# Kernel tuning notes

Hardware: AMD Instinct MI355X
Metric: run time of the kernel (lower is better)

## Reference

```python
import jax, jax.numpy as jnp
import numpy as np

B, D, L = 16, 256, 200
T = 1000   # max_frame_length
K = 3      # kernel_size
DW, DC = 4, 2


def setup_inputs() -> dict:
    key = jax.random.key(0)
    ks = jax.random.split(key, 16)
    plen = jax.random.randint(ks[0], (B,), 150, L + 1)
    pm = jnp.arange(L)[None, :] < plen[:, None]              # (B,L) True=valid
    phoneme_mask = pm[:, None, :]                            # (B,1,L)
    durations = jax.random.uniform(ks[1], (B, L), minval=1.0, maxval=8.0) * pm
    phoneme = jax.random.normal(ks[2], (B, D, L), dtype=jnp.float32)
    s = 0.05
    params = {
        'Wpw': jax.random.normal(ks[3], (D, D)) * s, 'bpw': jnp.zeros((D,)),
        'Cw': jax.random.normal(ks[4], (8, D, K)) * s, 'cbw': jnp.zeros((8,)),
        'Mw': jax.random.normal(ks[5], (10, DW)) * s, 'mbw': jnp.zeros((DW,)),
        'Lw': jax.random.normal(ks[6], (DW * D, D)) * s, 'lbw': jnp.zeros((D,)),
        'Wpc': jax.random.normal(ks[7], (D, D)) * s, 'bpc': jnp.zeros((D,)),
        'Cc': jax.random.normal(ks[8], (8, D, K)) * s, 'cbc': jnp.zeros((8,)),
        'Mc': jax.random.normal(ks[9], (10, DC)) * s, 'mbc': jnp.zeros((DC,)),
        'Lc': jax.random.normal(ks[10], (DW * DC, D)) * s, 'lbc': jnp.zeros((D,)),
        'Wo': jax.random.normal(ks[11], (D, 2 * D)) * s, 'bo': jnp.zeros((2 * D,)),
    }
    return {'durations': durations, 'phoneme': phoneme, 'phoneme_mask': phoneme_mask, **params}


def _conv_swish(x, W1, b1, Ck, cb, pm):
    # 1x1 conv (proj) then kernel-K 'same' conv then SiLU; mask padded phones
    h = jnp.einsum('od,bdl->bol', W1, x) + b1[None, :, None]
    h = jax.lax.conv_general_dilated(h, Ck, (1,), 'SAME',
                                     dimension_numbers=('NCH', 'OIH', 'NCH')) + cb[None, :, None]
    h = jax.nn.silu(h)
    h = jnp.where(pm[:, None, :], h, 0.0)
    return h.transpose(0, 2, 1)  # (B, L, 8)


def _mlp(S, E, h, M, mb):
    # concat start/end boundary scalars with per-phone conv features -> (B,T,L,10)
    feat = jnp.concatenate([S[..., None], E[..., None],
                            jnp.broadcast_to(h[:, None], (B, T, L, 8))], axis=-1)
    return jax.nn.silu(feat @ M + mb)


def _forward(durations, phoneme, phoneme_mask, Wpw, bpw, Cw, cbw, Mw, mbw, Lw, lbw,
             Wpc, bpc, Cc, cbc, Mc, mbc, Lc, lbc, Wo, bo):
    pm = phoneme_mask[:, 0, :]                                          # (B,L)
    frame_lengths = jnp.clip(jnp.round(durations.sum(-1)).astype(jnp.int32), 0, T)
    frame_mask = jnp.arange(T)[None, :] < frame_lengths[:, None]        # (B,T)
    attn_mask = frame_mask[:, :, None] & pm[:, None, :]                 # (B,T,L)
    sd = jnp.cumsum(durations, axis=-1)                                 # (B,L)
    sk = sd - durations
    t = jnp.arange(1, T + 1, dtype=durations.dtype)
    S = jnp.where(attn_mask, t[None, :, None] - sk[:, None, :], 0.0)    # (B,T,L)
    E = jnp.where(attn_mask, (sd - sk)[:, None, :], 0.0)                # (B,T,L)

    h_w = _conv_swish(phoneme, Wpw, bpw, Cw, cbw, pm)
    w = _mlp(S, E, h_w, Mw, mbw)                                        # (B,T,L,DW)
    w = jnp.where(pm[:, None, :, None], w, -jnp.inf)
    w = jax.nn.softmax(w, axis=2)                                       # softmax over phones
    w = jnp.where(frame_mask[:, :, None, None], w, 0.0)

    h_c = _conv_swish(phoneme, Wpc, bpc, Cc, cbc, pm)
    c = _mlp(S, E, h_c, Mc, mbc)                                        # (B,T,L,DC)

    wh = jnp.einsum('btlq,bdl->btqd', w, phoneme).reshape(B, T, DW * D) @ Lw + lbw
    wc = jnp.einsum('btlq,btlp->btqp', w, c).reshape(B, T, DW * DC) @ Lc + lbc
    whc = jnp.where(frame_mask[..., None], wh + wc, 0.0)                # (B,T,D)
    out = (whc @ Wo + bo).transpose(0, 2, 1)                            # (B,2D,T)
    return out, frame_mask, frame_lengths, w.transpose(0, 3, 1, 2)


def reference(durations, phoneme, phoneme_mask, Wpw, bpw, Cw, cbw, Mw, mbw, Lw, lbw,
              Wpc, bpc, Cc, cbc, Mc, mbc, Lc, lbc, Wo, bo):
    out, frame_mask, frame_lengths, w = _forward(
        durations, phoneme, phoneme_mask, Wpw, bpw, Cw, cbw, Mw, mbw, Lw, lbw,
        Wpc, bpc, Cc, cbc, Mc, mbc, Lc, lbc, Wo, bo)
    mean, log_std = jnp.split(out, 2, axis=1)                           # (B,D,T) each
    return (mean, log_std, frame_mask, frame_lengths, w)
```

## Files before the change

### kernel.cpp

```cpp
#include <hip/hip_runtime.h>
#include <hip/hip_bf16.h>
#include <math.h>

#define NB 16
#define ND 256
#define NL 200
#define NT 1000

typedef unsigned short ushort_t;
typedef __bf16 bf16x8 __attribute__((ext_vector_type(8)));
typedef float f32x4 __attribute__((ext_vector_type(4)));

#define LDS_AS(p) ((__attribute__((address_space(3))) void*)(p))
#define GLB_AS(p) ((const __attribute__((address_space(1))) void*)(p))

#define OFF_PHT   0u
#define OFF_SK    4966400u
#define OFF_EW    4969600u
#define OFF_EC    4975744u
#define OFF_BW2   4981888u
#define OFF_BC2   4981912u
#define OFF_FL    4981936u
#define OFF_GT    11535552u
#define OFF_WOT   15221952u
#define OFF_BASE  15287488u
#define OFF_PHTB  15320256u
#define OFF_LWT   15844544u

__device__ __forceinline__ float silu_f(float x){ return x / (1.f + __expf(-x)); }
__device__ __forceinline__ ushort_t f2bf(float x){
  __hip_bfloat16 h = __float2bfloat16(x);
  return *(ushort_t*)&h;
}

__global__ __launch_bounds__(256) void k_stage1(
    const float* __restrict__ dur, const float* __restrict__ ph,
    const float* __restrict__ Wp_w, const float* __restrict__ C_w, const float* __restrict__ bp_w,
    const float* __restrict__ Wp_c, const float* __restrict__ C_c, const float* __restrict__ bp_c,
    const float* __restrict__ Wo, const float* __restrict__ Lw,
    float* __restrict__ sk_ws, int* __restrict__ fl_ws,
    float* __restrict__ o_fm, float* __restrict__ o_fl,
    float* __restrict__ Ew, float* __restrict__ Ec,
    float* __restrict__ bw2, float* __restrict__ bc2,
    ushort_t* __restrict__ WoT, ushort_t* __restrict__ LwT,
    float* __restrict__ phT, ushort_t* __restrict__ phTb)
{
  int bid = blockIdx.x, tid = threadIdx.x;
  if (bid < 16){
    int b = bid;
    __shared__ float sdur[NL];
    __shared__ float ssk[NL];
    __shared__ int sfl;
    if (tid < NL) sdur[tid] = dur[b*NL + tid];
    __syncthreads();
    if (tid == 0){
      float run = 0.f;
      for (int l = 0; l < NL; ++l){ ssk[l] = run; run += sdur[l]; }
      int fl = (int)rintf(run);
      fl = fl < 0 ? 0 : (fl > NT ? NT : fl);
      sfl = fl; fl_ws[b] = fl; o_fl[b] = (float)fl;
    }
    __syncthreads();
    if (tid < NL) sk_ws[b*NL + tid] = ssk[tid];
    for (int t = tid; t < NT; t += 256) o_fm[b*NT + t] = (t < sfl) ? 1.f : 0.f;
  } else if (bid < 1600){
    int sbid = bid - 16;
    if (sbid < 48){
      int gid = sbid*256 + tid;
      int branch = gid / 6144;
      int r = gid % 6144;
      int d = r & 255;
      int ock = r >> 8;
      int oc = ock / 3, k = ock % 3;
      const float* Wp = branch ? Wp_c : Wp_w;
      const float* C  = branch ? C_c  : C_w;
      float acc = 0.f;
      for (int i = 0; i < ND; ++i) acc += C[(oc*ND + i)*3 + k] * Wp[i*ND + d];
      (branch ? Ec : Ew)[r] = acc;
      if (d == 0){
        const float* bp = branch ? bp_c : bp_w;
        float bb = 0.f;
        for (int i = 0; i < ND; ++i) bb += C[(oc*ND + i)*3 + k] * bp[i];
        (branch ? bc2 : bw2)[ock] = bb;
      }
    } else {
      int gid = (sbid - 48)*256 + tid;
      if (gid < 131072){
        int n = gid >> 8, k = gid & 255;
        WoT[gid] = f2bf(Wo[(size_t)k*512 + n]);
      } else {
        int r = gid - 131072;
        int d = r & 255;
        int qn = r >> 8;
        int q = qn >> 8, n = qn & 255;
        LwT[r] = f2bf(Lw[((size_t)q*256 + d)*256 + n]);
      }
    }
  } else {
    int r = bid - 1600;
    int xb = r & 7, yb = (r >> 3) & 7, b = r >> 6;
    int l0 = xb*32, d0 = yb*32;
    int tx = tid & 31, ty = tid >> 5;
    __shared__ float tile[32][33];
    #pragma unroll
    for (int i = 0; i < 4; ++i){
      int d = d0 + ty + i*8, l = l0 + tx;
      tile[ty + i*8][tx] = (l < NL) ? ph[((size_t)b*ND + d)*NL + l] : 0.f;
    }
    __syncthreads();
    #pragma unroll
    for (int i = 0; i < 4; ++i){
      int l = l0 + ty + i*8, d = d0 + tx;
      float v = tile[tx][ty + i*8];
      if (l < NL) phT[((size_t)b*NL + l)*ND + d] = v;
      phTb[((size_t)b*256 + l)*ND + d] = f2bf(v);
    }
  }
}

__global__ __launch_bounds__(256) void k_stage2(
    const float* __restrict__ phT,
    const float* __restrict__ dur, const float* __restrict__ sk_ws,
    const float* __restrict__ Ew, const float* __restrict__ Ec,
    const float* __restrict__ bw2, const float* __restrict__ bc2,
    const float* __restrict__ cbw, const float* __restrict__ cbc,
    const float* __restrict__ Mw, const float* __restrict__ mbw,
    const float* __restrict__ Mc, const float* __restrict__ mbc,
    float4* __restrict__ base,
    const ushort_t* __restrict__ LwT, const ushort_t* __restrict__ phTb,
    ushort_t* __restrict__ Gt)
{
  int bid = blockIdx.x, tid = threadIdx.x;
  if (bid < 256){
    int b = bid >> 4, x = bid & 15;
    if (x >= 13){
      int l0 = 208 + (x - 13)*16;
      if (tid < 32)
        base[((size_t)(b*256 + l0 + (tid >> 1)))*2 + (tid & 1)] = make_float4(0,0,0,0);
      return;
    }
    __shared__ float sh[16][17];
    int lu = tid >> 4, u = tid & 15;
    int l = x*16 + lu;
    float h = 0.f;
    if (l < NL){
      int branch = u >> 3, oc = u & 7;
      const float* E  = branch ? Ec  : Ew;
      const float* b2 = branch ? bc2 : bw2;
      float val = (branch ? cbc : cbw)[oc];
      #pragma unroll
      for (int k = 0; k < 3; ++k){
        int ll = l + k - 1;
        if (ll < 0 || ll >= NL) continue;
        float acc = b2[oc*3 + k];
        const float4* Er = (const float4*)(E + (oc*3 + k)*ND);
        const float4* pr = (const float4*)(phT + ((size_t)b*NL + ll)*ND);
        #pragma unroll 8
        for (int d = 0; d < 64; ++d){
          float4 e = Er[d], p = pr[d];
          acc += e.x*p.x + e.y*p.y + e.z*p.z + e.w*p.w;
        }
        val += acc;
      }
      float pm = (dur[b*NL + l] > 0.5f) ? 1.f : 0.f;
      h = silu_f(val) * pm;
    }
    sh[lu][u] = h;
    __syncthreads();
    if (tid < 16){
      int ll = x*16 + tid;
      float4 o0 = make_float4(0,0,0,0);
      float4 o1 = make_float4(0,0,0,0);
      if (ll < NL){
        float dl  = dur[b*NL + ll];
        float pm  = (dl > 0.5f) ? 1.f : 0.f;
        float skl = sk_ws[b*NL + ll];
        float c1[4], c2[2];
        #pragma unroll
        for (int q = 0; q < 4; ++q) c1[q] = mbw[q] + dl*Mw[4 + q] - skl*Mw[q];
        #pragma unroll
        for (int p = 0; p < 2; ++p) c2[p] = mbc[p] + dl*Mc[2 + p] - skl*Mc[p];
        #pragma unroll
        for (int j = 0; j < 8; ++j){
          float hwv = sh[tid][j], hcv = sh[tid][8 + j];
          #pragma unroll
          for (int q = 0; q < 4; ++q) c1[q] += hwv*Mw[(2 + j)*4 + q];
          #pragma unroll
          for (int p = 0; p < 2; ++p) c2[p] += hcv*Mc[(2 + j)*2 + p];
        }
        o0 = make_float4(c1[0], c1[1], c1[2], c1[3]);
        o1 = make_float4(c2[0], c2[1], pm, 0.f);
      }
      base[((size_t)(b*256 + ll))*2 + 0] = o0;
      base[((size_t)(b*256 + ll))*2 + 1] = o1;
    }
  } else {
    int r = bid - 256;
    int xb = r & 1, yb = (r >> 1) & 1, bq = r >> 2;
    int b = bq >> 2, q = bq & 3;
    int m0 = yb * 128;
    int n0 = xb * 128;
    __shared__ ushort_t As[4096];
    __shared__ ushort_t Bs[4096];
    int lane = tid & 63, wave = tid >> 6;
    int wm = wave >> 1, wn = wave & 1;
    int col = lane & 15, kg4 = lane >> 4;
    f32x4 acc[4][4] = {};
    for (int kt = 0; kt < 8; ++kt){
      int k0 = kt*32;
      #pragma unroll
      for (int rr = 0; rr < 2; ++rr){
        int o = wave*1024 + rr*4096;
        int co = o + (lane << 4);
        int kg = co >> 11, row = (co >> 4) & 127;
        const ushort_t* ga = LwT + ((size_t)(q*256 + m0 + row))*256 + k0 + kg*8;
        __builtin_amdgcn_global_load_lds(GLB_AS(ga), LDS_AS(As + (o >> 1)), 16, 0, 0);
        const ushort_t* gb = phTb + ((size_t)(b*256 + n0 + row))*256 + k0 + kg*8;
        __builtin_amdgcn_global_load_lds(GLB_AS(gb), LDS_AS(Bs + (o >> 1)), 16, 0, 0);
      }
      __builtin_amdgcn_s_waitcnt(0);
      __syncthreads();
      const bf16x8* Av = (const bf16x8*)As;
      const bf16x8* Bv = (const bf16x8*)Bs;
      bf16x8 afr[4], bfr[4];
      #pragma unroll
      for (int i = 0; i < 4; ++i) afr[i] = Av[kg4*128 + wm*64 + i*16 + col];
      #pragma unroll
      for (int j = 0; j < 4; ++j) bfr[j] = Bv[kg4*128 + wn*64 + j*16 + col];
      #pragma unroll
      for (int i = 0; i < 4; ++i)
        #pragma unroll
        for (int j = 0; j < 4; ++j)
          acc[i][j] = __builtin_amdgcn_mfma_f32_16x16x32_bf16(afr[i], bfr[j], acc[i][j], 0, 0, 0);
      __syncthreads();
    }
    int rq = lane >> 4;
    #pragma unroll
    for (int i = 0; i < 4; ++i){
      #pragma unroll
      for (int rr = 0; rr < 4; ++rr){
        int n = m0 + wm*64 + i*16 + rq*4 + rr;
        #pragma unroll
        for (int j = 0; j < 4; ++j){
          int l = n0 + wn*64 + j*16 + col;
          if (l < NL)
            Gt[((size_t)b*ND + n)*800 + q*NL + l] = f2bf(acc[i][j][rr]);
        }
      }
    }
  }
}

#define AP 808
#define WP 264
__global__ __launch_bounds__(256) void k_wvo(
    const float4* __restrict__ base,
    const int* __restrict__ fl_ws,
    const float* __restrict__ Mw, const float* __restrict__ Mc,
    const ushort_t* __restrict__ Gt,
    const ushort_t* __restrict__ WoT,
    const float* __restrict__ Lc,
    const float* __restrict__ lbc,
    const float* __restrict__ lbw,
    const float* __restrict__ bo,
    float* __restrict__ wout,
    float* __restrict__ o_mean, float* __restrict__ o_lstd)
{
  __shared__ ushort_t As[16*AP];
  __shared__ ushort_t Bs[8192];
  __shared__ ushort_t whcs[16*WP];
  __shared__ float    wcs[16][8];
  int b = blockIdx.y;
  int m0 = blockIdx.x * 16;
  int tid = threadIdx.x, lane = tid & 63, wave = tid >> 6;
  int col = lane & 15, kg4 = lane >> 4, quad = lane >> 4;
  int fl = fl_ws[b];

  for (int s = 0; s < 4; ++s){
    int tl = wave*4 + s;
    int t = m0 + tl;
    if (t >= fl){
      for (int k = lane; k < 800; k += 64) As[tl*AP + k] = 0;
      if (lane < 8) wcs[tl][lane] = 0.f;
      if (t < NT){
        #pragma unroll
        for (int q = 0; q < 4; ++q)
          #pragma unroll
          for (int c = 0; c < 4; ++c){
            int l = c*64 + lane;
            if (l < NL) wout[(((size_t)(b*4 + q))*NT + t)*NL + l] = 0.f;
          }
      }
      continue;
    }
    float t1 = (float)(t + 1);
    float tqw[4], tqc[2];
    #pragma unroll
    for (int q = 0; q < 4; ++q) tqw[q] = t1 * Mw[q];
    #pragma unroll
    for (int p = 0; p < 2; ++p) tqc[p] = t1 * Mc[p];
    float z[4][4], cv[4][2], msk[4];
    float m[4] = {-INFINITY, -INFINITY, -INFINITY, -INFINITY};
    #pragma unroll
    for (int c = 0; c < 4; ++c){
      int l = c*64 + lane;
      float4 b0 = base[((size_t)(b*256 + l))*2 + 0];
      float4 b1 = base[((size_t)(b*256 + l))*2 + 1];
      float pm = b1.z;
      msk[c] = pm;
      float zz[4] = { b0.x + tqw[0], b0.y + tqw[1], b0.z + tqw[2], b0.w + tqw[3] };
      #pragma unroll
      for (int q = 0; q < 4; ++q){
        float sv = silu_f(zz[q]);
        z[c][q] = (pm > 0.f) ? sv : -INFINITY;
        m[q] = fmaxf(m[q], z[c][q]);
      }
      cv[c][0] = silu_f(b1.x + tqc[0]);
      cv[c][1] = silu_f(b1.y + tqc[1]);
    }
    #pragma unroll
    for (int q = 0; q < 4; ++q){
      float v = m[q];
      #pragma unroll
      for (int off = 32; off; off >>= 1) v = fmaxf(v, __shfl_xor(v, off));
      m[q] = v;
    }
    float s4[4] = {0,0,0,0};
    #pragma unroll
    for (int c = 0; c < 4; ++c){
      #pragma unroll
      for (int q = 0; q < 4; ++q){
        float e = (msk[c] > 0.f) ? __expf(z[c][q] - m[q]) : 0.f;
        z[c][q] = e;
        s4[q] += e;
      }
    }
    #pragma unroll
    for (int q = 0; q < 4; ++q){
      float v = s4[q];
      #pragma unroll
      for (int off = 32; off; off >>= 1) v += __shfl_xor(v, off);
      s4[q] = 1.f / v;
    }
    float wc[8] = {0,0,0,0,0,0,0,0};
    #pragma unroll
    for (int c = 0; c < 4; ++c){
      int l = c*64 + lane;
      bool lv = l < NL;
      #pragma unroll
      for (int q = 0; q < 4; ++q){
        float wq = z[c][q] * s4[q];
        if (lv){
          wout[(((size_t)(b*4 + q))*NT + t)*NL + l] = wq;
          As[tl*AP + q*NL + l] = f2bf(wq);
        }
        wc[q*2 + 0] += wq * cv[c][0];
        wc[q*2 + 1] += wq * cv[c][1];
      }
    }
    #pragma unroll
    for (int u = 0; u < 8; ++u){
      float v = wc[u];
      #pragma unroll
      for (int off = 32; off; off >>= 1) v += __shfl_xor(v, off);
      wc[u] = v;
    }
    if (lane == 0){
      #pragma unroll
      for (int u = 0; u < 8; ++u) wcs[tl][u] = wc[u];
    }
  }
  __syncthreads();

  f32x4 accv[4] = {};
  for (int kt = 0; kt < 25; ++kt){
    int k0 = kt*32;
    #pragma unroll
    for (int r = 0; r < 4; ++r){
      int o = (wave*4 + r) << 10;
      int co = o + (lane << 4);
      int kg = co >> 12, row = (co >> 4) & 255;
      const ushort_t* gb = Gt + ((size_t)(b*ND + row))*800 + k0 + kg*8;
      __builtin_amdgcn_global_load_lds(GLB_AS(gb), LDS_AS(Bs + (co >> 1)), 16, 0, 0);
    }
    __builtin_amdgcn_s_waitcnt(0);
    __syncthreads();
    const bf16x8* Bv = (const bf16x8*)Bs;
    bf16x8 afr = *(const bf16x8*)(&As[col*AP + k0 + kg4*8]);
    bf16x8 bfr[4];
    #pragma unroll
    for (int j = 0; j < 4; ++j) bfr[j] = Bv[kg4*256 + wave*64 + j*16 + col];
    #pragma unroll
    for (int j = 0; j < 4; ++j)
      accv[j] = __builtin_amdgcn_mfma_f32_16x16x32_bf16(afr, bfr[j], accv[j], 0, 0, 0);
    __syncthreads();
  }

  #pragma unroll
  for (int j = 0; j < 4; ++j){
    int n = wave*64 + j*16 + col;
    float lbn = lbc[n], lbwn = lbw[n];
    float lc0 = Lc[0*ND+n], lc1 = Lc[1*ND+n], lc2 = Lc[2*ND+n], lc3 = Lc[3*ND+n];
    float lc4 = Lc[4*ND+n], lc5 = Lc[5*ND+n], lc6 = Lc[6*ND+n], lc7 = Lc[7*ND+n];
    #pragma unroll
    for (int r = 0; r < 4; ++r){
      int tl = quad*4 + r;
      float f = (m0 + tl < fl) ? 1.f : 0.f;
      float vcv = lbn
        + wcs[tl][0]*lc0 + wcs[tl][1]*lc1 + wcs[tl][2]*lc2 + wcs[tl][3]*lc3
        + wcs[tl][4]*lc4 + wcs[tl][5]*lc5 + wcs[tl][6]*lc6 + wcs[tl][7]*lc7;
      whcs[tl*WP + n] = f2bf(f * (accv[j][r] + lbwn + vcv));
    }
  }
  __syncthreads();

  f32x4 acco[8] = {};
  for (int kt = 0; kt < 8; ++kt){
    int k0 = kt*32;
    bf16x8 bfr = *(const bf16x8*)(&whcs[col*WP + k0 + kg4*8]);
    #pragma unroll
    for (int i = 0; i < 8; ++i){
      bf16x8 afr = *(const bf16x8*)(WoT + ((size_t)(wave*128 + i*16 + col))*ND + k0 + kg4*8);
      acco[i] = __builtin_amdgcn_mfma_f32_16x16x32_bf16(afr, bfr, acco[i], 0, 0, 0);
    }
  }
  int t = m0 + col;
  if (t < NT){
    #pragma unroll
    for (int i = 0; i < 8; ++i){
      #pragma unroll
      for (int r = 0; r < 4; ++r){
        int s = wave*128 + i*16 + quad*4 + r;
        float v = acco[i][r] + bo[s];
        if (s < ND) o_mean[((size_t)b*ND + s)*NT + t] = v;
        else        o_lstd[((size_t)b*ND + (s - ND))*NT + t] = v;
      }
    }
  }
}

extern "C" void kernel_launch(void* const* d_in, const int* in_sizes, int n_in,
                              void* d_out, int out_size, void* d_ws, size_t ws_size,
                              hipStream_t stream)
{
  const float* dur = (const float*)d_in[0];
  const float* ph  = (const float*)d_in[1];
  const float* Wpw = (const float*)d_in[3];
  const float* bpw = (const float*)d_in[4];
  const float* Cw  = (const float*)d_in[5];
  const float* cbw = (const float*)d_in[6];
  const float* Mw  = (const float*)d_in[7];
  const float* mbw = (const float*)d_in[8];
  const float* Lw  = (const float*)d_in[9];
  const float* lbw = (const float*)d_in[10];
  const float* Wpc = (const float*)d_in[11];
  const float* bpc = (const float*)d_in[12];
  const float* Cc  = (const float*)d_in[13];
  const float* cbc = (const float*)d_in[14];
  const float* Mc  = (const float*)d_in[15];
  const float* mbc = (const float*)d_in[16];
  const float* Lc  = (const float*)d_in[17];
  const float* lbc = (const float*)d_in[18];
  const float* Wo  = (const float*)d_in[19];
  const float* bo  = (const float*)d_in[20];

  float* out    = (float*)d_out;
  float* o_mean = out;
  float* o_lstd = out + (size_t)NB*ND*NT;
  float* o_fm   = o_lstd + (size_t)NB*ND*NT;
  float* o_fl   = o_fm + NB*NT;
  float* o_w    = o_fl + NB;

  float* ws   = (float*)d_ws;
  float* phT  = ws + OFF_PHT;
  float* sk   = ws + OFF_SK;
  float* Ew   = ws + OFF_EW;
  float* Ec   = ws + OFF_EC;
  float* bw2  = ws + OFF_BW2;
  float* bc2  = ws + OFF_BC2;
  int*   fl   = (int*)(ws + OFF_FL);
  ushort_t* Gt   = (ushort_t*)(ws + OFF_GT);
  ushort_t* WoT  = (ushort_t*)(ws + OFF_WOT);
  float4*   base = (float4*)(ws + OFF_BASE);
  ushort_t* phTb = (ushort_t*)(ws + OFF_PHTB);
  ushort_t* LwT  = (ushort_t*)(ws + OFF_LWT);

  k_stage1<<<2624, 256, 0, stream>>>(dur, ph, Wpw, Cw, bpw, Wpc, Cc, bpc, Wo, Lw,
                                     sk, fl, o_fm, o_fl, Ew, Ec, bw2, bc2,
                                     WoT, LwT, phT, phTb);
  k_stage2<<<320, 256, 0, stream>>>(phT, dur, sk, Ew, Ec, bw2, bc2, cbw, cbc,
                                    Mw, mbw, Mc, mbc, base, LwT, phTb, Gt);
  {
    dim3 g(64, NB);
    k_wvo<<<g, 256, 0, stream>>>(base, fl, Mw, Mc, Gt, WoT, Lc, lbc, lbw, bo,
                                 o_w, o_mean, o_lstd);
  }
}
```

Before: 280.4 us.

## Split output projection into separate tiled MFMA GEMM kernel via workspace

Moves the final whc @ Wo projection out of the fused k_wvo kernel into a standalone 128x128-tiled bf16 MFMA GEMM over all B*T rows. whc is written to a global workspace buffer, and the new kernel stages WoT and whc tiles through LDS with direct global-to-LDS loads. The fused version reloaded WoT from global for every 16-frame block; tiling gives much more reuse. The cost is an extra kernel launch and a round trip of whc through global memory.

```diff
diff --git a/kernel.cpp b/kernel.cpp
--- a/kernel.cpp
+++ b/kernel.cpp
@@ -22,6 +22,7 @@
 #define OFF_BC2   4981912u
 #define OFF_FL    4981936u
 #define OFF_GT    11535552u
+#define OFF_WHC   13173952u
 #define OFF_WOT   15221952u
 #define OFF_BASE  15287488u
 #define OFF_PHTB  15320256u
@@ -252,23 +253,19 @@
 }
 
 #define AP 808
-#define WP 264
-__global__ __launch_bounds__(256) void k_wvo(
+__global__ __launch_bounds__(256) void k_wv(
     const float4* __restrict__ base,
     const int* __restrict__ fl_ws,
     const float* __restrict__ Mw, const float* __restrict__ Mc,
     const ushort_t* __restrict__ Gt,
-    const ushort_t* __restrict__ WoT,
     const float* __restrict__ Lc,
     const float* __restrict__ lbc,
     const float* __restrict__ lbw,
-    const float* __restrict__ bo,
     float* __restrict__ wout,
-    float* __restrict__ o_mean, float* __restrict__ o_lstd)
+    ushort_t* __restrict__ whc)
 {
   __shared__ ushort_t As[16*AP];
   __shared__ ushort_t Bs[8192];
-  __shared__ ushort_t whcs[16*WP];
   __shared__ float    wcs[16][8];
   int b = blockIdx.y;
   int m0 = blockIdx.x * 16;
@@ -405,33 +402,74 @@
     #pragma unroll
     for (int r = 0; r < 4; ++r){
       int tl = quad*4 + r;
-      float f = (m0 + tl < fl) ? 1.f : 0.f;
+      int t = m0 + tl;
+      if (t >= NT) continue;
+      float f = (t < fl) ? 1.f : 0.f;
       float vcv = lbn
         + wcs[tl][0]*lc0 + wcs[tl][1]*lc1 + wcs[tl][2]*lc2 + wcs[tl][3]*lc3
         + wcs[tl][4]*lc4 + wcs[tl][5]*lc5 + wcs[tl][6]*lc6 + wcs[tl][7]*lc7;
-      whcs[tl*WP + n] = f2bf(f * (accv[j][r] + lbwn + vcv));
-    }
-  }
-  __syncthreads();
-
-  f32x4 acco[8] = {};
+      whc[((size_t)b*NT + t)*ND + n] = f2bf(f * (accv[j][r] + lbwn + vcv));
+    }
+  }
+}
+
+__global__ __launch_bounds__(256) void k_gemmO_mfma(
+    const ushort_t* __restrict__ whc,
+    const ushort_t* __restrict__ WoT,
+    const float* __restrict__ bo,
+    float* __restrict__ o_mean, float* __restrict__ o_lstd)
+{
+  __shared__ ushort_t As[4096];
+  __shared__ ushort_t Bs[4096];
+  int m0 = blockIdx.y * 128;
+  int n0 = blockIdx.x * 128;
+  int tid = threadIdx.x, lane = tid & 63, wave = tid >> 6;
+  int wm = wave >> 1, wn = wave & 1;
+  int col = lane & 15, kg4 = lane >> 4;
+
+  f32x4 acc[4][4] = {};
+
   for (int kt = 0; kt < 8; ++kt){
     int k0 = kt*32;
-    bf16x8 bfr = *(const bf16x8*)(&whcs[col*WP + k0 + kg4*8]);
-    #pragma unroll
-    for (int i = 0; i < 8; ++i){
-      bf16x8 afr = *(const bf16x8*)(WoT + ((size_t)(wave*128 + i*16 + col))*ND + k0 + kg4*8);
-      acco[i] = __builtin_amdgcn_mfma_f32_16x16x32_bf16(afr, bfr, acco[i], 0, 0, 0);
-    }
-  }
-  int t = m0 + col;
-  if (t < NT){
-    #pragma unroll
-    for (int i = 0; i < 8; ++i){
-      #pragma unroll
-      for (int r = 0; r < 4; ++r){
-        int s = wave*128 + i*16 + quad*4 + r;
-        float v = acco[i][r] + bo[s];
+    #pragma unroll
+    for (int r = 0; r < 2; ++r){
+      int o = wave*1024 + r*4096;
+      int co = o + (lane << 4);
+      int kg = co >> 11, row = (co >> 4) & 127;
+      const ushort_t* ga = WoT + ((size_t)(m0 + row))*ND + k0 + kg*8;
+      __builtin_amdgcn_global_load_lds(GLB_AS(ga), LDS_AS(As + (o >> 1)), 16, 0, 0);
+      const ushort_t* gb = whc + ((size_t)(n0 + row))*ND + k0 + kg*8;
+      __builtin_amdgcn_global_load_lds(GLB_AS(gb), LDS_AS(Bs + (o >> 1)), 16, 0, 0);
+    }
+    __builtin_amdgcn_s_waitcnt(0);
+    __syncthreads();
+    const bf16x8* Av = (const bf16x8*)As;
+    const bf16x8* Bv = (const bf16x8*)Bs;
+    bf16x8 afr[4], bfr[4];
+    #pragma unroll
+    for (int i = 0; i < 4; ++i) afr[i] = Av[kg4*128 + wm*64 + i*16 + col];
+    #pragma unroll
+    for (int j = 0; j < 4; ++j) bfr[j] = Bv[kg4*128 + wn*64 + j*16 + col];
+    #pragma unroll
+    for (int i = 0; i < 4; ++i)
+      #pragma unroll
+      for (int j = 0; j < 4; ++j)
+        acc[i][j] = __builtin_amdgcn_mfma_f32_16x16x32_bf16(afr[i], bfr[j], acc[i][j], 0, 0, 0);
+    __syncthreads();
+  }
+
+  int rq = lane >> 4;
+  #pragma unroll
+  for (int i = 0; i < 4; ++i){
+    #pragma unroll
+    for (int r = 0; r < 4; ++r){
+      int s = m0 + wm*64 + i*16 + rq*4 + r;
+      float bov = bo[s];
+      #pragma unroll
+      for (int j = 0; j < 4; ++j){
+        int bt = n0 + wn*64 + j*16 + col;
+        int b = bt / NT, t = bt - b*NT;
+        float v = acc[i][j][r] + bov;
         if (s < ND) o_mean[((size_t)b*ND + s)*NT + t] = v;
         else        o_lstd[((size_t)b*ND + (s - ND))*NT + t] = v;
       }
@@ -480,6 +518,7 @@
   float* bc2  = ws + OFF_BC2;
   int*   fl   = (int*)(ws + OFF_FL);
   ushort_t* Gt   = (ushort_t*)(ws + OFF_GT);
+  ushort_t* whc  = (ushort_t*)(ws + OFF_WHC);
   ushort_t* WoT  = (ushort_t*)(ws + OFF_WOT);
   float4*   base = (float4*)(ws + OFF_BASE);
   ushort_t* phTb = (ushort_t*)(ws + OFF_PHTB);
@@ -492,7 +531,10 @@
                                     Mw, mbw, Mc, mbc, base, LwT, phTb, Gt);
   {
     dim3 g(64, NB);
-    k_wvo<<<g, 256, 0, stream>>>(base, fl, Mw, Mc, Gt, WoT, Lc, lbc, lbw, bo,
-                                 o_w, o_mean, o_lstd);
+    k_wv<<<g, 256, 0, stream>>>(base, fl, Mw, Mc, Gt, Lc, lbc, lbw, o_w, whc);
+  }
+  {
+    dim3 g(125, 4);
+    k_gemmO_mfma<<<g, 256, 0, stream>>>(whc, WoT, bo, o_mean, o_lstd);
   }
 }
```

Measured after the change: 266.5 us. 5.0% less time.
